# Kernel optimization log

Hardware: AMD Instinct MI355X
Metric: run time of the kernel (lower is better)

## Reference

```python
import jax, jax.numpy as jnp
import numpy as np

B, T, I, H, L, O = 64, 1024, 256, 512, 2, 256


def setup_inputs() -> dict:
    key = jax.random.key(0)
    ks = jax.random.split(key, 12)
    s = 1.0 / np.sqrt(H)  # PyTorch RNN init scale
    return {
        "x": jax.random.normal(ks[0], (B, T, I), jnp.float32),
        "W_ih0": jax.random.normal(ks[1], (3 * H, I), jnp.float32) * s,
        "W_hh0": jax.random.normal(ks[2], (3 * H, H), jnp.float32) * s,
        "b_ih0": jax.random.normal(ks[3], (3 * H,), jnp.float32) * s,
        "b_hh0": jax.random.normal(ks[4], (3 * H,), jnp.float32) * s,
        "W_ih1": jax.random.normal(ks[5], (3 * H, H), jnp.float32) * s,
        "W_hh1": jax.random.normal(ks[6], (3 * H, H), jnp.float32) * s,
        "b_ih1": jax.random.normal(ks[7], (3 * H,), jnp.float32) * s,
        "b_hh1": jax.random.normal(ks[8], (3 * H,), jnp.float32) * s,
        "fc_w": jax.random.normal(ks[9], (O, H), jnp.float32) * s,
        "fc_b": jax.random.normal(ks[10], (O,), jnp.float32) * s,
    }


def gru_layer(x, W_ih, W_hh, b_ih, b_hh):
    """One PyTorch-convention GRU layer, batch_first input [B,T,*], h0=0."""
    Bt, Tt, _ = x.shape
    Hh = W_hh.shape[1]
    # Precompute input-side gate pre-activations for all timesteps: [T,B,3H]
    xg = (jnp.einsum('bti,gi->btg', x, W_ih) + b_ih).transpose(1, 0, 2)

    def step(h, xg_t):
        hg = h @ W_hh.T + b_hh                      # [B,3H]
        xr, xz, xn = jnp.split(xg_t, 3, axis=-1)
        hr, hz, hn = jnp.split(hg, 3, axis=-1)
        r = jax.nn.sigmoid(xr + hr)
        z = jax.nn.sigmoid(xz + hz)
        n = jnp.tanh(xn + r * hn)
        h_new = (1.0 - z) * n + z * h
        return h_new, h_new

    h0 = jnp.zeros((Bt, Hh), x.dtype)
    hT, hs = jax.lax.scan(step, h0, xg)
    return hs.transpose(1, 0, 2), hT  # [B,T,H], [B,H]


def reference(x, W_ih0, W_hh0, b_ih0, b_hh0, W_ih1, W_hh1, b_ih1, b_hh1, fc_w, fc_b):
    out0, h0 = gru_layer(x, W_ih0, W_hh0, b_ih0, b_hh0)
    out1, h1 = gru_layer(out0, W_ih1, W_hh1, b_ih1, b_hh1)
    hidden = jnp.stack([h0, h1], axis=0)            # [num_layers, B, H]
    flat = out1.reshape(-1, out1.shape[-1])          # [B*T, H]
    out = flat @ fc_w.T + fc_b                       # [B*T, O]
    return out, hidden
```

## Files before the change

kernel.cpp:

```cpp
#include <hip/hip_runtime.h>
#include <hip/hip_bf16.h>
#include <hip/hip_fp16.h>
#include <stdint.h>
#include <type_traits>

#define B_ 64
#define T_ 1024
#define I_ 256
#define H_ 512
#define G3_ 1536
#define O_ 256

typedef __attribute__((ext_vector_type(4))) float floatx4;
typedef __attribute__((ext_vector_type(8))) short short8;
typedef __attribute__((ext_vector_type(2))) _Float16 half2v;

#define BARX() __asm__ volatile("s_waitcnt lgkmcnt(0)\n\ts_barrier" ::: "memory")

static __device__ __forceinline__ float fdot2f(uint32_t a, uint32_t b, float c) {
#if __has_builtin(__builtin_amdgcn_fdot2)
  return __builtin_amdgcn_fdot2(__builtin_bit_cast(half2v, a),
                                __builtin_bit_cast(half2v, b), c, false);
#else
  __half2 ha = __builtin_bit_cast(__half2, a);
  __half2 hb = __builtin_bit_cast(__half2, b);
  float2 fa = __half22float2(ha), fb = __half22float2(hb);
  return c + fa.x * fb.x + fa.y * fb.y;
#endif
}

static __device__ __forceinline__ float sigmoid_f(float x) {
  float e = __expf(-fabsf(x));
  float a = 1.f / (1.f + e);
  return x >= 0.f ? a : 1.f - a;
}
static __device__ __forceinline__ float tanh_f(float x) {
  float e = __expf(-2.f * fabsf(x));
  float a = (1.f - e) / (1.f + e);
  return x >= 0.f ? a : -a;
}
static __device__ __forceinline__ uint32_t pack_h2(float a, float b) {
  return (uint32_t)__half_as_ushort(__float2half(a)) |
         ((uint32_t)__half_as_ushort(__float2half(b)) << 16);
}
static __device__ __forceinline__ uint32_t pack_bf2(float a, float b) {
  return (uint32_t)__builtin_bit_cast(unsigned short, __float2bfloat16(a)) |
         ((uint32_t)__builtin_bit_cast(unsigned short, __float2bfloat16(b)) << 16);
}

__global__ void init_kernel(const float* __restrict__ Whh0, const float* __restrict__ Whh1,
                            const float* __restrict__ bih0, const float* __restrict__ bhh0,
                            const float* __restrict__ bih1, const float* __restrict__ bhh1,
                            uint32_t* __restrict__ wpack, float* __restrict__ biasv,
                            uint32_t* __restrict__ hstate) {
  int idx = blockIdx.x * 256 + threadIdx.x;
  if (idx < 786432) {
    int l = idx / 393216, rem = idx % 393216;
    int j = rem & 127;
    int g = (rem >> 7) % 3;
    int kk = (rem / 384) & 63;
    int s = (rem / 24576) & 3;
    int c = rem / 98304;
    const float* W = l ? Whh1 : Whh0;
    int row = g * 512 + c * 128 + j;
    int k = s * 128 + kk * 2;
    uint32_t lo = __half_as_ushort(__float2half(W[(size_t)row * 512 + k]));
    uint32_t hi = __half_as_ushort(__float2half(W[(size_t)row * 512 + k + 1]));
    wpack[idx] = lo | (hi << 16);
  }
  int i2 = idx - 786432;
  if (i2 >= 0 && i2 < 3072) {
    int l = i2 / 1536, n = i2 % 1536;
    const float* bi = l ? bih1 : bih0;
    const float* bh = l ? bhh1 : bhh0;
    biasv[i2] = bi[n] + (n < 1024 ? bh[n] : 0.f);
  }
  int i3 = idx - (786432 + 3072);
  if (i3 >= 0 && i3 < 32768) hstate[i3] = 0u;
}

template <typename TA, typename TC>
__global__ __launch_bounds__(256, 2) void gemm_bt(
    const TA* __restrict__ A, const float* __restrict__ Bw,
    const float* __restrict__ bias, TC* __restrict__ C,
    int K, int lda, int ldc, int tcshift, int t0, int Ttot) {
  __shared__ unsigned short As[128 * 40];
  __shared__ unsigned short Bs[128 * 40];
  const int tid = threadIdx.x;
  const int bm = blockIdx.x, bn = blockIdx.y;
  const int r = tid >> 1, hf = tid & 1;

  const int m = bm * 128 + r;
  const long arow = (long)(m >> tcshift) * Ttot + t0 + (m & ((1 << tcshift) - 1));
  const TA* ap = A + arow * (long)lda + hf * 16;
  const int n = bn * 128 + r;
  const float* bp = Bw + (long)n * K + hf * 16;

  const int wid = tid >> 6, lane = tid & 63;
  const int wm = (wid >> 1) * 64, wn = (wid & 1) * 64;
  const int m16 = lane & 15, quad = lane >> 4;

  floatx4 acc[4][4];
#pragma unroll
  for (int i = 0; i < 4; ++i)
#pragma unroll
    for (int j = 0; j < 4; ++j) acc[i][j] = 0.f;

  for (int k0 = 0; k0 < K; k0 += 32) {
    unsigned short ta[16], tb[16];
    if constexpr (std::is_same<TA, float>::value) {
      const float4* p = (const float4*)(ap + k0);
#pragma unroll
      for (int q = 0; q < 4; ++q) {
        float4 v = p[q];
        ta[q * 4 + 0] = __builtin_bit_cast(unsigned short, __float2bfloat16(v.x));
        ta[q * 4 + 1] = __builtin_bit_cast(unsigned short, __float2bfloat16(v.y));
        ta[q * 4 + 2] = __builtin_bit_cast(unsigned short, __float2bfloat16(v.z));
        ta[q * 4 + 3] = __builtin_bit_cast(unsigned short, __float2bfloat16(v.w));
      }
    } else {
      const uint4* p = (const uint4*)(ap + k0);
      *(uint4*)&ta[0] = p[0];
      *(uint4*)&ta[8] = p[1];
    }
    {
      const float4* p = (const float4*)(bp + k0);
#pragma unroll
      for (int q = 0; q < 4; ++q) {
        float4 v = p[q];
        tb[q * 4 + 0] = __builtin_bit_cast(unsigned short, __float2bfloat16(v.x));
        tb[q * 4 + 1] = __builtin_bit_cast(unsigned short, __float2bfloat16(v.y));
        tb[q * 4 + 2] = __builtin_bit_cast(unsigned short, __float2bfloat16(v.z));
        tb[q * 4 + 3] = __builtin_bit_cast(unsigned short, __float2bfloat16(v.w));
      }
    }
    *(uint4*)&As[r * 40 + hf * 16] = *(uint4*)&ta[0];
    *(uint4*)&As[r * 40 + hf * 16 + 8] = *(uint4*)&ta[8];
    *(uint4*)&Bs[r * 40 + hf * 16] = *(uint4*)&tb[0];
    *(uint4*)&Bs[r * 40 + hf * 16 + 8] = *(uint4*)&tb[8];
    __syncthreads();
    short8 af[4], bfr[4];
#pragma unroll
    for (int mt = 0; mt < 4; ++mt)
      af[mt] = *(const short8*)&As[(wm + mt * 16 + m16) * 40 + quad * 8];
#pragma unroll
    for (int nt = 0; nt < 4; ++nt)
      bfr[nt] = *(const short8*)&Bs[(wn + nt * 16 + m16) * 40 + quad * 8];
#pragma unroll
    for (int mt = 0; mt < 4; ++mt)
#pragma unroll
      for (int nt = 0; nt < 4; ++nt)
        acc[mt][nt] = __builtin_amdgcn_mfma_f32_16x16x32_bf16(af[mt], bfr[nt],
                                                              acc[mt][nt], 0, 0, 0);
    __syncthreads();
  }
#pragma unroll
  for (int mt = 0; mt < 4; ++mt)
#pragma unroll
    for (int nt = 0; nt < 4; ++nt)
#pragma unroll
      for (int rr = 0; rr < 4; ++rr) {
        int grow = bm * 128 + wm + mt * 16 + quad * 4 + rr;
        int gcol = bn * 128 + wn + nt * 16 + m16;
        float v = acc[mt][nt][rr];
        if (bias) v += bias[gcol];
        if constexpr (std::is_same<TC, float>::value)
          C[(long)grow * ldc + gcol] = v;
        else
          C[(long)grow * ldc + gcol] = __float2half(v);
      }
}

__global__ __launch_bounds__(512, 2) void gru_rec(
    const uint32_t* __restrict__ wpack, const uint32_t* __restrict__ xgd,
    const float* __restrict__ bhh, uint32_t* __restrict__ hstate,
    uint32_t* __restrict__ outw, uint64_t* __restrict__ pkts,
    float* __restrict__ hid_out,
    int t0, int Tc, int outT, int outT0, int last) {
  const int tid = threadIdx.x;
  const int wave = tid >> 6, lane = tid & 63;
  const int s = tid >> 7;
  const int b = blockIdx.x & 63;
  const int c = blockIdx.x >> 6;

  __shared__ uint32_t hds[256];
  __shared__ float part[3][512];
  __shared__ uint32_t xbuf[3][64];

  uint32_t w[192];
  {
    const uint32_t* wp = wpack + (size_t)(c * 4 + s) * 24576 + (tid & 127);
#pragma unroll
    for (int i = 0; i < 192; ++i) w[i] = wp[(size_t)i * 128];
  }

  if (tid < 256) hds[tid] = hstate[b * 256 + tid];

  uint32_t xp0 = 0, xp1 = 0, xp2 = 0;
  if (wave == 1) {
    size_t base = ((size_t)b * Tc) * 768 + c * 64 + lane;
    xp0 = xgd[base];
    xp1 = xgd[base + 256];
    xp2 = xgd[base + 512];
  }
  float hold0 = 0.f, hold1 = 0.f, bn0 = 0.f, bn1 = 0.f;
  if (wave == 0) {
    uint32_t hv = hstate[b * 256 + c * 64 + lane];
    __half2 hh = __builtin_bit_cast(__half2, hv);
    hold0 = __half2float(hh.x);
    hold1 = __half2float(hh.y);
    bn0 = bhh[1024 + c * 128 + 2 * lane];
    bn1 = bhh[1024 + c * 128 + 2 * lane + 1];
  }
  BARX();

  for (int tt = 0; tt < Tc; ++tt) {
    const int t = t0 + tt;
    const uint32_t tagv = (uint32_t)(t + 1);
    const int slot = t & 1;

    if (wave == 1) {
      xbuf[0][lane] = xp0;
      xbuf[1][lane] = xp1;
      xbuf[2][lane] = xp2;
      if (tt + 1 < Tc) {
        size_t base = ((size_t)b * Tc + tt + 1) * 768 + c * 64 + lane;
        xp0 = xgd[base];
        xp1 = xgd[base + 256];
        xp2 = xgd[base + 512];
      }
    }
    float ar = 0.f, az = 0.f, an = 0.f;
    const int hb = s * 64;
#pragma unroll
    for (int k4 = 0; k4 < 16; ++k4) {
      uint4 u4 = *((const uint4*)&hds[hb] + k4);
      ar = fdot2f(w[(k4 * 4 + 0) * 3 + 0], u4.x, ar);
      az = fdot2f(w[(k4 * 4 + 0) * 3 + 1], u4.x, az);
      an = fdot2f(w[(k4 * 4 + 0) * 3 + 2], u4.x, an);
      ar = fdot2f(w[(k4 * 4 + 1) * 3 + 0], u4.y, ar);
      az = fdot2f(w[(k4 * 4 + 1) * 3 + 1], u4.y, az);
      an = fdot2f(w[(k4 * 4 + 1) * 3 + 2], u4.y, an);
      ar = fdot2f(w[(k4 * 4 + 2) * 3 + 0], u4.z, ar);
      az = fdot2f(w[(k4 * 4 + 2) * 3 + 1], u4.z, az);
      an = fdot2f(w[(k4 * 4 + 2) * 3 + 2], u4.z, an);
      ar = fdot2f(w[(k4 * 4 + 3) * 3 + 0], u4.w, ar);
      az = fdot2f(w[(k4 * 4 + 3) * 3 + 1], u4.w, az);
      an = fdot2f(w[(k4 * 4 + 3) * 3 + 2], u4.w, an);
    }
    part[0][tid] = ar;
    part[1][tid] = az;
    part[2][tid] = an;
    BARX();

    if (wave == 0) {
      float hr0 = 0.f, hz0 = 0.f, hn0 = 0.f, hr1 = 0.f, hz1 = 0.f, hn1 = 0.f;
#pragma unroll
      for (int ss = 0; ss < 4; ++ss) {
        float2 vr = *(const float2*)&part[0][ss * 128 + 2 * lane];
        float2 vz = *(const float2*)&part[1][ss * 128 + 2 * lane];
        float2 vn = *(const float2*)&part[2][ss * 128 + 2 * lane];
        hr0 += vr.x; hr1 += vr.y;
        hz0 += vz.x; hz1 += vz.y;
        hn0 += vn.x; hn1 += vn.y;
      }
      __half2 xr = __builtin_bit_cast(__half2, xbuf[0][lane]);
      __half2 xz = __builtin_bit_cast(__half2, xbuf[1][lane]);
      __half2 xn = __builtin_bit_cast(__half2, xbuf[2][lane]);
      float r0 = sigmoid_f(__half2float(xr.x) + hr0);
      float r1 = sigmoid_f(__half2float(xr.y) + hr1);
      float z0 = sigmoid_f(__half2float(xz.x) + hz0);
      float z1 = sigmoid_f(__half2float(xz.y) + hz1);
      float n0 = tanh_f(__half2float(xn.x) + r0 * (hn0 + bn0));
      float n1 = tanh_f(__half2float(xn.y) + r1 * (hn1 + bn1));
      float h0 = (1.f - z0) * n0 + z0 * hold0;
      float h1 = (1.f - z1) * n1 + z1 * hold1;
      hold0 = h0;
      hold1 = h1;
      uint32_t hd = pack_h2(h0, h1);
      hds[c * 64 + lane] = hd;
      uint64_t pk = (uint64_t)hd | ((uint64_t)tagv << 32);
      __hip_atomic_store(&pkts[(((size_t)slot * 64 + b) * 4 + c) * 64 + lane], pk,
                         __ATOMIC_RELAXED, __HIP_MEMORY_SCOPE_AGENT);
      outw[((size_t)b * outT + outT0 + tt) * 256 + c * 64 + lane] = pack_bf2(h0, h1);
    }
    if (wave >= 4) {
      int cc = wave - 4;
      if (cc != c) {
        const uint64_t* pp = &pkts[(((size_t)slot * 64 + b) * 4 + cc) * 64 + lane];
        uint64_t v;
        do {
          v = __hip_atomic_load(pp, __ATOMIC_RELAXED, __HIP_MEMORY_SCOPE_AGENT);
        } while ((uint32_t)(v >> 32) != tagv);
        hds[cc * 64 + lane] = (uint32_t)v;
      }
    }
    BARX();
  }

  if (tid < 256) hstate[b * 256 + tid] = hds[tid];
  if (last && tid < 128) {
    int jp = c * 128 + tid;
    hid_out[b * 512 + jp] = __half2float(((const __half*)hds)[jp]);
  }
}

extern "C" void kernel_launch(void* const* d_in, const int* in_sizes, int n_in,
                              void* d_out, int out_size, void* d_ws, size_t ws_size,
                              hipStream_t stream) {
  const float* x = (const float*)d_in[0];
  const float* W_ih0 = (const float*)d_in[1];
  const float* W_hh0 = (const float*)d_in[2];
  const float* b_ih0 = (const float*)d_in[3];
  const float* b_hh0 = (const float*)d_in[4];
  const float* W_ih1 = (const float*)d_in[5];
  const float* W_hh1 = (const float*)d_in[6];
  const float* b_ih1 = (const float*)d_in[7];
  const float* b_hh1 = (const float*)d_in[8];
  const float* fc_w = (const float*)d_in[9];
  const float* fc_b = (const float*)d_in[10];
  float* out = (float*)d_out;

  char* p = (char*)d_ws;
  size_t off = 0;
  auto alloc = [&](size_t bytes) -> void* {
    void* r = p + off;
    off = (off + bytes + 255) & ~(size_t)255;
    return r;
  };
  uint32_t* wpack = (uint32_t*)alloc((size_t)786432 * 4);
  float* biasv = (float*)alloc((size_t)3072 * 4);
  uint32_t* hstate = (uint32_t*)alloc((size_t)32768 * 4);
  uint64_t* pkts = (uint64_t*)alloc((size_t)2 * 2 * 64 * 4 * 64 * 8);
  __hip_bfloat16* out1 = (__hip_bfloat16*)alloc((size_t)B_ * T_ * H_ * 2);

  int Tc = 1024;
  while (Tc > 64) {
    size_t need = (size_t)B_ * Tc * H_ * 2 + (size_t)B_ * Tc * G3_ * 2 + 1024;
    if (off + need <= ws_size) break;
    Tc >>= 1;
  }
  __hip_bfloat16* out0c = (__hip_bfloat16*)alloc((size_t)B_ * Tc * H_ * 2);
  __half* xg = (__half*)alloc((size_t)B_ * Tc * G3_ * 2);
  int tcs = __builtin_ctz(Tc);

  init_kernel<<<3212, 256, 0, stream>>>(W_hh0, W_hh1, b_ih0, b_hh0, b_ih1, b_hh1,
                                        wpack, biasv, hstate);

  for (int t0 = 0; t0 < 1024; t0 += Tc) {
    const int M = B_ * Tc;
    const int last = (t0 + Tc) == 1024;
    {
      dim3 gg(M / 128, G3_ / 128);
      gemm_bt<float, __half><<<gg, 256, 0, stream>>>(x, W_ih0, biasv, xg, I_, I_,
                                                     G3_, tcs, t0, 1024);
      gru_rec<<<256, 512, 0, stream>>>(wpack, (const uint32_t*)xg, b_hh0, hstate,
                                       (uint32_t*)out0c, pkts,
                                       out + 16777216, t0, Tc, Tc, 0, last);
    }
    {
      dim3 gg(M / 128, G3_ / 128);
      gemm_bt<__hip_bfloat16, __half><<<gg, 256, 0, stream>>>(
          out0c, W_ih1, biasv + 1536, xg, H_, H_, G3_, tcs, 0, Tc);
      gru_rec<<<256, 512, 0, stream>>>(wpack + 393216, (const uint32_t*)xg, b_hh1,
                                       hstate + 16384, (uint32_t*)out1,
                                       pkts + 32768,
                                       out + 16777216 + 32768, t0, Tc, 1024, t0, last);
    }
  }
  dim3 gf(65536 / 128, O_ / 128);
  gemm_bt<__hip_bfloat16, float><<<gf, 256, 0, stream>>>(out1, fc_w, fc_b, out,
                                                         H_, H_, O_, 10, 0, 1024);
}
```

Before: 4.416 ms.

## Poll hidden-state packets per slice and drop second per-step barrier

```diff
diff --git a/kernel.cpp b/kernel.cpp
--- a/kernel.cpp
+++ b/kernel.cpp
@@ -183,9 +183,8 @@
   const int b = blockIdx.x & 63;
   const int c = blockIdx.x >> 6;
 
-  __shared__ uint32_t hds[256];
-  __shared__ float part[3][512];
-  __shared__ uint32_t xbuf[3][64];
+  __shared__ uint32_t hbw[4][64];
+  __shared__ float part[2][3][512];
 
   uint32_t w[192];
   {
@@ -194,16 +193,8 @@
     for (int i = 0; i < 192; ++i) w[i] = wp[(size_t)i * 128];
   }
 
-  if (tid < 256) hds[tid] = hstate[b * 256 + tid];
-
-  uint32_t xp0 = 0, xp1 = 0, xp2 = 0;
-  if (wave == 1) {
-    size_t base = ((size_t)b * Tc) * 768 + c * 64 + lane;
-    xp0 = xgd[base];
-    xp1 = xgd[base + 256];
-    xp2 = xgd[base + 512];
-  }
   float hold0 = 0.f, hold1 = 0.f, bn0 = 0.f, bn1 = 0.f;
+  uint32_t xrw = 0, xzw = 0, xnw = 0;
   if (wave == 0) {
     uint32_t hv = hstate[b * 256 + c * 64 + lane];
     __half2 hh = __builtin_bit_cast(__half2, hv);
@@ -211,30 +202,30 @@
     hold1 = __half2float(hh.y);
     bn0 = bhh[1024 + c * 128 + 2 * lane];
     bn1 = bhh[1024 + c * 128 + 2 * lane + 1];
-  }
-  BARX();
+    size_t base = ((size_t)b * Tc) * 768 + c * 64 + lane;
+    xrw = xgd[base];
+    xzw = xgd[base + 256];
+    xnw = xgd[base + 512];
+  }
 
   for (int tt = 0; tt < Tc; ++tt) {
     const int t = t0 + tt;
-    const uint32_t tagv = (uint32_t)(t + 1);
-    const int slot = t & 1;
-
-    if (wave == 1) {
-      xbuf[0][lane] = xp0;
-      xbuf[1][lane] = xp1;
-      xbuf[2][lane] = xp2;
-      if (tt + 1 < Tc) {
-        size_t base = ((size_t)b * Tc + tt + 1) * 768 + c * 64 + lane;
-        xp0 = xgd[base];
-        xp1 = xgd[base + 256];
-        xp2 = xgd[base + 512];
-      }
-    }
+    uint32_t hp;
+    if (tt == 0) {
+      hp = hstate[b * 256 + s * 64 + lane];
+    } else {
+      const uint64_t* pp = &pkts[(((size_t)(t & 1)) * 64 + b) * 256 + s * 64 + lane];
+      uint64_t v;
+      do {
+        v = __hip_atomic_load(pp, __ATOMIC_RELAXED, __HIP_MEMORY_SCOPE_AGENT);
+      } while ((uint32_t)(v >> 32) != (uint32_t)t);
+      hp = (uint32_t)v;
+    }
+    hbw[s][lane] = hp;
     float ar = 0.f, az = 0.f, an = 0.f;
-    const int hb = s * 64;
 #pragma unroll
     for (int k4 = 0; k4 < 16; ++k4) {
-      uint4 u4 = *((const uint4*)&hds[hb] + k4);
+      uint4 u4 = *((const uint4*)&hbw[s][0] + k4);
       ar = fdot2f(w[(k4 * 4 + 0) * 3 + 0], u4.x, ar);
       az = fdot2f(w[(k4 * 4 + 0) * 3 + 1], u4.x, az);
       an = fdot2f(w[(k4 * 4 + 0) * 3 + 2], u4.x, an);
@@ -248,25 +239,26 @@
       az = fdot2f(w[(k4 * 4 + 3) * 3 + 1], u4.w, az);
       an = fdot2f(w[(k4 * 4 + 3) * 3 + 2], u4.w, an);
     }
-    part[0][tid] = ar;
-    part[1][tid] = az;
-    part[2][tid] = an;
+    const int ps = t & 1;
+    part[ps][0][tid] = ar;
+    part[ps][1][tid] = az;
+    part[ps][2][tid] = an;
     BARX();
 
     if (wave == 0) {
       float hr0 = 0.f, hz0 = 0.f, hn0 = 0.f, hr1 = 0.f, hz1 = 0.f, hn1 = 0.f;
 #pragma unroll
       for (int ss = 0; ss < 4; ++ss) {
-        float2 vr = *(const float2*)&part[0][ss * 128 + 2 * lane];
-        float2 vz = *(const float2*)&part[1][ss * 128 + 2 * lane];
-        float2 vn = *(const float2*)&part[2][ss * 128 + 2 * lane];
+        float2 vr = *(const float2*)&part[ps][0][ss * 128 + 2 * lane];
+        float2 vz = *(const float2*)&part[ps][1][ss * 128 + 2 * lane];
+        float2 vn = *(const float2*)&part[ps][2][ss * 128 + 2 * lane];
         hr0 += vr.x; hr1 += vr.y;
         hz0 += vz.x; hz1 += vz.y;
         hn0 += vn.x; hn1 += vn.y;
       }
-      __half2 xr = __builtin_bit_cast(__half2, xbuf[0][lane]);
-      __half2 xz = __builtin_bit_cast(__half2, xbuf[1][lane]);
-      __half2 xn = __builtin_bit_cast(__half2, xbuf[2][lane]);
+      __half2 xr = __builtin_bit_cast(__half2, xrw);
+      __half2 xz = __builtin_bit_cast(__half2, xzw);
+      __half2 xn = __builtin_bit_cast(__half2, xnw);
       float r0 = sigmoid_f(__half2float(xr.x) + hr0);
       float r1 = sigmoid_f(__half2float(xr.y) + hr1);
       float z0 = sigmoid_f(__half2float(xz.x) + hz0);
@@ -278,30 +270,25 @@
       hold0 = h0;
       hold1 = h1;
       uint32_t hd = pack_h2(h0, h1);
-      hds[c * 64 + lane] = hd;
-      uint64_t pk = (uint64_t)hd | ((uint64_t)tagv << 32);
-      __hip_atomic_store(&pkts[(((size_t)slot * 64 + b) * 4 + c) * 64 + lane], pk,
-                         __ATOMIC_RELAXED, __HIP_MEMORY_SCOPE_AGENT);
+      uint64_t pk = (uint64_t)hd | ((uint64_t)(uint32_t)(t + 1) << 32);
+      __hip_atomic_store(&pkts[(((size_t)((t + 1) & 1)) * 64 + b) * 256 + c * 64 + lane],
+                         pk, __ATOMIC_RELAXED, __HIP_MEMORY_SCOPE_AGENT);
       outw[((size_t)b * outT + outT0 + tt) * 256 + c * 64 + lane] = pack_bf2(h0, h1);
-    }
-    if (wave >= 4) {
-      int cc = wave - 4;
-      if (cc != c) {
-        const uint64_t* pp = &pkts[(((size_t)slot * 64 + b) * 4 + cc) * 64 + lane];
-        uint64_t v;
-        do {
-          v = __hip_atomic_load(pp, __ATOMIC_RELAXED, __HIP_MEMORY_SCOPE_AGENT);
-        } while ((uint32_t)(v >> 32) != tagv);
-        hds[cc * 64 + lane] = (uint32_t)v;
-      }
-    }
-    BARX();
-  }
-
-  if (tid < 256) hstate[b * 256 + tid] = hds[tid];
-  if (last && tid < 128) {
-    int jp = c * 128 + tid;
-    hid_out[b * 512 + jp] = __half2float(((const __half*)hds)[jp]);
+      if (tt + 1 < Tc) {
+        size_t base = ((size_t)b * Tc + tt + 1) * 768 + c * 64 + lane;
+        xrw = xgd[base];
+        xzw = xgd[base + 256];
+        xnw = xgd[base + 512];
+      }
+    }
+  }
+
+  if (wave == 0) {
+    hstate[b * 256 + c * 64 + lane] = pack_h2(hold0, hold1);
+    if (last) {
+      float2 hv = make_float2(hold0, hold1);
+      *(float2*)&hid_out[b * 512 + c * 128 + 2 * lane] = hv;
+    }
   }
 }
 
```

New measurement: 4.398 ms. About the same (-0.4%).
